# Kernel optimization log

Measured on AMD Instinct MI355X. Metric: run time of the kernel, lower is better.

The kernel has to match this reference:

```python
import jax, jax.numpy as jnp
import numpy as np
import math

B, S, E = 8, 128, 192
H = 6
HD = E // H  # 32
L = 64       # latent_dim (hardcoded default in MHLA)
N_EXP = 8
TOP_K = 2
ED = 768     # expert_dim
EPS = 1e-5


def setup_inputs() -> dict:
    key = jax.random.key(0)
    ks = jax.random.split(key, 24)
    sc = 0.02
    nrm = lambda k, shp: (jax.random.normal(k, shp, dtype=jnp.float32) * sc)
    inp = {
        "x": jax.random.normal(ks[0], (B, S, E), dtype=jnp.float32),
        "rms1_w": jnp.ones((E,), jnp.float32),
        "rms2_w": jnp.ones((E,), jnp.float32),
        # latent_tokens: Linear(S*E -> L*E); stored [in, out]
        "latW": nrm(ks[1], (S * E, L * E)),
        "latb": jnp.zeros((L * E,), jnp.float32),
        "qW": nrm(ks[2], (E, E)), "qb": jnp.zeros((E,), jnp.float32),
        "kW": nrm(ks[3], (E, E)), "kb": jnp.zeros((E,), jnp.float32),
        "vW": nrm(ks[4], (E, E)), "vb": jnp.zeros((E,), jnp.float32),
        "oW": nrm(ks[5], (E, E)), "ob": jnp.zeros((E,), jnp.float32),
        "rW": nrm(ks[6], (E, N_EXP)), "rb": jnp.zeros((N_EXP,), jnp.float32),
        # stacked expert params: layer1 (E->ED), swiglu-linear (ED->ED), layer2 (ED->E)
        "e1W": nrm(ks[7], (N_EXP, E, ED)), "e1b": jnp.zeros((N_EXP, ED), jnp.float32),
        "swW": nrm(ks[8], (N_EXP, ED, ED)), "swb": jnp.zeros((N_EXP, ED), jnp.float32),
        "e2W": nrm(ks[9], (N_EXP, ED, E)), "e2b": jnp.zeros((N_EXP, E), jnp.float32),
    }
    return inp


def _rmsnorm(x, w):
    ms = jnp.mean(x * x, axis=-1, keepdims=True)
    return x * jax.lax.rsqrt(ms + EPS) * w


def _rope_q(q):
    # q: [B,H,S,HD]; rotate interleaved pairs, torch-style view(..., HD//2, 2)
    t = jnp.arange(S, dtype=jnp.float32)
    inv_freq = 1.0 / (10000.0 ** (jnp.arange(0, HD, 2, dtype=jnp.float32) / HD))
    freqs = jnp.outer(t, inv_freq)            # [S, HD/2]
    cos, sin = jnp.cos(freqs), jnp.sin(freqs)
    qp = q.reshape(B, H, S, HD // 2, 2)
    x1, x2 = qp[..., 0], qp[..., 1]
    r1 = x1 * cos - x2 * sin
    r2 = x1 * sin + x2 * cos
    return jnp.stack([r1, r2], axis=-1).reshape(B, H, S, HD)


def _mhla(x, latW, latb, qW, qb, kW, kb, vW, vb, oW, ob):
    latent = (x.reshape(B, S * E) @ latW + latb).reshape(B, L, E)
    q = (x @ qW + qb).reshape(B, S, H, HD).transpose(0, 2, 1, 3)       # [B,H,S,HD]
    k = (latent @ kW + kb).reshape(B, L, H, HD).transpose(0, 2, 1, 3)  # [B,H,L,HD]
    v = (latent @ vW + vb).reshape(B, L, H, HD).transpose(0, 2, 1, 3)
    qr = _rope_q(q)  # RoPE applied to query only (key_r = key in source)
    scores = jnp.einsum("bhsd,bhld->bhsl", qr, k) / math.sqrt(HD)
    attn = jax.nn.softmax(scores, axis=-1)
    out = jnp.einsum("bhsl,bhld->bhsd", attn, v)
    out = out.transpose(0, 2, 1, 3).reshape(B, S, E)
    return out @ oW + ob


def _moe(h, rW, rb, e1W, e1b, swW, swb, e2W, e2b):
    probs = jax.nn.softmax(h @ rW + rb, axis=-1)          # [B,S,N]
    pk, idx = jax.lax.top_k(probs, TOP_K)                 # [B,S,K]
    # dense all-expert compute (8 small experts), then gather top-k
    t1 = jnp.einsum("bse,neh->bsnh", h, e1W) + e1b        # [B,S,N,ED]
    t2 = jax.nn.relu(jnp.einsum("bsnh,nhg->bsng", t1, swW) + swb)
    eo = jnp.einsum("bsng,nge->bsne", t2, e2W) + e2b      # [B,S,N,E]
    sel = jnp.take_along_axis(eo, idx[..., None], axis=2) # [B,S,K,E]
    return jnp.sum(pk[..., None] * sel, axis=2)


def reference(x, rms1_w, rms2_w, latW, latb, qW, qb, kW, kb, vW, vb, oW, ob,
              rW, rb, e1W, e1b, swW, swb, e2W, e2b):
    x = x + _mhla(_rmsnorm(x, rms1_w), latW, latb, qW, qb, kW, kb, vW, vb, oW, ob)
    x = x + _moe(_rmsnorm(x, rms2_w), rW, rb, e1W, e1b, swW, swb, e2W, e2b)
    return x
```

## Files before the change

### kernel.cpp

```cpp
#include <hip/hip_runtime.h>
#include <hip/hip_bf16.h>
#include <math.h>

#define B 8
#define S 128
#define E 192
#define H 6
#define HD 32
#define L 64
#define NEXP 8
#define ED 768
#define T (B*S)
#define SE (S*E)
#define LE (L*E)

#define SPLITS 64
#define ISPAN 384
#define CHUNK 128

using s8 = __attribute__((ext_vector_type(8))) short;
using f4 = __attribute__((ext_vector_type(4))) float;

__global__ __launch_bounds__(64) void rmsnorm_k(const float* __restrict__ x,
                                                const float* __restrict__ w,
                                                float* __restrict__ y) {
  int row = blockIdx.x;
  int lane = threadIdx.x;
  const float* xr = x + (size_t)row * E;
  float v0 = xr[lane], v1 = xr[lane + 64], v2 = xr[lane + 128];
  float s = v0 * v0 + v1 * v1 + v2 * v2;
#pragma unroll
  for (int off = 32; off > 0; off >>= 1) s += __shfl_xor(s, off);
  float inv = rsqrtf(s * (1.0f / E) + 1e-5f);
  float* yr = y + (size_t)row * E;
  yr[lane]       = v0 * inv * w[lane];
  yr[lane + 64]  = v1 * inv * w[lane + 64];
  yr[lane + 128] = v2 * inv * w[lane + 128];
}

__global__ __launch_bounds__(256) void lat_partial_k(const float* __restrict__ xn,
                                                     const float* __restrict__ latW,
                                                     float* __restrict__ part) {
  const int tid = threadIdx.x;
  const int j = blockIdx.x * 1024 + tid * 4;
  const int i0 = blockIdx.y * ISPAN;
  __shared__ float xs[CHUNK][8];
  f4 acc[8];
#pragma unroll
  for (int b = 0; b < 8; ++b) acc[b] = (f4){0.f, 0.f, 0.f, 0.f};
  for (int c = 0; c < ISPAN; c += CHUNK) {
    float* xsf = (float*)xs;
    __syncthreads();
    for (int l = tid; l < CHUNK * 8; l += 256) {
      int ii = l >> 3, b = l & 7;
      xsf[l] = xn[(size_t)b * SE + i0 + c + ii];
    }
    __syncthreads();
#pragma unroll 8
    for (int ii = 0; ii < CHUNK; ++ii) {
      const f4 w = __builtin_nontemporal_load(
          (const f4*)&latW[(size_t)(i0 + c + ii) * LE + j]);
#pragma unroll
      for (int b = 0; b < 8; ++b) {
        float xv = xs[ii][b];
        acc[b][0] += xv * w[0];
        acc[b][1] += xv * w[1];
        acc[b][2] += xv * w[2];
        acc[b][3] += xv * w[3];
      }
    }
  }
#pragma unroll
  for (int b = 0; b < 8; ++b)
    *(f4*)&part[((size_t)blockIdx.y * 8 + b) * LE + j] = acc[b];
}

__global__ __launch_bounds__(256) void lat_reduce_k(const float* __restrict__ part,
                                                    const float* __restrict__ latb,
                                                    float* __restrict__ lat) {
  int g = blockIdx.x * 256 + threadIdx.x;
  int b = g / LE, j = g - b * LE;
  float s = latb[j];
  for (int sp = 0; sp < SPLITS; ++sp) s += part[((size_t)sp * 8 + b) * LE + j];
  lat[g] = s;
}

__global__ __launch_bounds__(256) void qkv_k(const float* __restrict__ xn,
                                             const float* __restrict__ lat,
                                             const float* __restrict__ qW, const float* __restrict__ qb,
                                             const float* __restrict__ kW, const float* __restrict__ kb,
                                             const float* __restrict__ vW, const float* __restrict__ vb,
                                             float* __restrict__ qo,
                                             float* __restrict__ ko,
                                             float* __restrict__ vo) {
  const int z = blockIdx.z;
  const float* A = (z == 0) ? xn : lat;
  const float* W = (z == 0) ? qW : (z == 1) ? kW : vW;
  const float* bp = (z == 0) ? qb : (z == 1) ? kb : vb;
  float* C = (z == 0) ? qo : (z == 1) ? ko : vo;
  const int M = (z == 0) ? T : (B * L);
  const int m0 = blockIdx.y * 64;
  if (m0 >= M) return;
  const int n0 = blockIdx.x * 64;
  __shared__ float As[16][64];
  __shared__ float Ws[16][64];
  const int tid = threadIdx.x;
  const int tx = tid & 15, ty = tid >> 4;
  const int arow = tid >> 2, acol = (tid & 3) << 2;
  const int wrow = tid >> 4, wcol = (tid & 15) << 2;
  float acc[4][4] = {{0.f}};
  for (int kb2 = 0; kb2 < E; kb2 += 16) {
    float4 a = *(const float4*)&A[(size_t)(m0 + arow) * E + kb2 + acol];
    As[acol][arow] = a.x;
    As[acol + 1][arow] = a.y;
    As[acol + 2][arow] = a.z;
    As[acol + 3][arow] = a.w;
    *(float4*)&Ws[wrow][wcol] = *(const float4*)&W[(size_t)(kb2 + wrow) * E + n0 + wcol];
    __syncthreads();
#pragma unroll
    for (int k = 0; k < 16; ++k) {
      float4 a4 = *(const float4*)&As[k][ty << 2];
      float4 w4 = *(const float4*)&Ws[k][tx << 2];
      acc[0][0] += a4.x * w4.x; acc[0][1] += a4.x * w4.y; acc[0][2] += a4.x * w4.z; acc[0][3] += a4.x * w4.w;
      acc[1][0] += a4.y * w4.x; acc[1][1] += a4.y * w4.y; acc[1][2] += a4.y * w4.z; acc[1][3] += a4.y * w4.w;
      acc[2][0] += a4.z * w4.x; acc[2][1] += a4.z * w4.y; acc[2][2] += a4.z * w4.z; acc[2][3] += a4.z * w4.w;
      acc[3][0] += a4.w * w4.x; acc[3][1] += a4.w * w4.y; acc[3][2] += a4.w * w4.z; acc[3][3] += a4.w * w4.w;
    }
    __syncthreads();
  }
#pragma unroll
  for (int i = 0; i < 4; ++i) {
    int m = m0 + (ty << 2) + i;
#pragma unroll
    for (int jj = 0; jj < 4; ++jj) {
      int n = n0 + (tx << 2) + jj;
      C[(size_t)m * E + n] = acc[i][jj] + bp[n];
    }
  }
}

__global__ __launch_bounds__(256) void gemm_k(const float* __restrict__ A,
                                              const float* __restrict__ W,
                                              const float* __restrict__ bias,
                                              const float* __restrict__ resid,
                                              float* __restrict__ C,
                                              int M, int N, int K,
                                              int flags) {
  const int n0 = blockIdx.x * 64;
  const int m0 = blockIdx.y * 64;
  __shared__ float As[16][64];
  __shared__ float Ws[16][64];
  const int tid = threadIdx.x;
  const int tx = tid & 15, ty = tid >> 4;
  const int arow = tid >> 2, acol = (tid & 3) << 2;
  const int wrow = tid >> 4, wcol = (tid & 15) << 2;
  float acc[4][4] = {{0.f}};
  for (int kb = 0; kb < K; kb += 16) {
    float4 a = *(const float4*)&A[(size_t)(m0 + arow) * K + kb + acol];
    As[acol][arow] = a.x;
    As[acol + 1][arow] = a.y;
    As[acol + 2][arow] = a.z;
    As[acol + 3][arow] = a.w;
    *(float4*)&Ws[wrow][wcol] = *(const float4*)&W[(size_t)(kb + wrow) * N + n0 + wcol];
    __syncthreads();
#pragma unroll
    for (int k = 0; k < 16; ++k) {
      float4 a4 = *(const float4*)&As[k][ty << 2];
      float4 w4 = *(const float4*)&Ws[k][tx << 2];
      acc[0][0] += a4.x * w4.x; acc[0][1] += a4.x * w4.y; acc[0][2] += a4.x * w4.z; acc[0][3] += a4.x * w4.w;
      acc[1][0] += a4.y * w4.x; acc[1][1] += a4.y * w4.y; acc[1][2] += a4.y * w4.z; acc[1][3] += a4.y * w4.w;
      acc[2][0] += a4.z * w4.x; acc[2][1] += a4.z * w4.y; acc[2][2] += a4.z * w4.z; acc[2][3] += a4.z * w4.w;
      acc[3][0] += a4.w * w4.x; acc[3][1] += a4.w * w4.y; acc[3][2] += a4.w * w4.z; acc[3][3] += a4.w * w4.w;
    }
    __syncthreads();
  }
#pragma unroll
  for (int i = 0; i < 4; ++i) {
    int m = m0 + (ty << 2) + i;
#pragma unroll
    for (int j = 0; j < 4; ++j) {
      int n = n0 + (tx << 2) + j;
      float v = acc[i][j];
      if (bias) v += bias[n];
      if (flags & 1) v = fmaxf(v, 0.f);
      if (flags & 2) v += resid[(size_t)m * N + n];
      C[(size_t)m * N + n] = v;
    }
  }
}

__global__ __launch_bounds__(256) void tconv_k(const float* __restrict__ in,
                                               __hip_bfloat16* __restrict__ out,
                                               int K, int N) {
  const int e = blockIdx.z;
  in += (size_t)e * K * N;
  out += (size_t)e * N * K;
  __shared__ float tile[32][33];
  int tx = threadIdx.x & 31, r8 = threadIdx.x >> 5;
  int k0 = blockIdx.x * 32, n0 = blockIdx.y * 32;
#pragma unroll
  for (int i = 0; i < 4; ++i)
    tile[r8 + 8 * i][tx] = in[(size_t)(k0 + r8 + 8 * i) * N + n0 + tx];
  __syncthreads();
#pragma unroll
  for (int i = 0; i < 4; ++i) {
    int nr = r8 + 8 * i;
    out[(size_t)(n0 + nr) * K + k0 + tx] = __float2bfloat16(tile[tx][nr]);
  }
}

__global__ __launch_bounds__(64) void router_rms_k(const float* __restrict__ x1,
                                                   const float* __restrict__ w,
                                                   const float* __restrict__ rW,
                                                   const float* __restrict__ rb,
                                                   __hip_bfloat16* __restrict__ hb,
                                                   float* __restrict__ pk,
                                                   int* __restrict__ idx) {
  int t = blockIdx.x;
  int lane = threadIdx.x;
  const float* xr = x1 + (size_t)t * E;
  float v0 = xr[lane], v1 = xr[lane + 64], v2 = xr[lane + 128];
  float s = v0 * v0 + v1 * v1 + v2 * v2;
#pragma unroll
  for (int off = 32; off > 0; off >>= 1) s += __shfl_xor(s, off);
  float inv = rsqrtf(s * (1.0f / E) + 1e-5f);
  float r0 = v0 * inv * w[lane];
  float r1 = v1 * inv * w[lane + 64];
  float r2 = v2 * inv * w[lane + 128];
  __hip_bfloat16* yrb = hb + (size_t)t * E;
  yrb[lane] = __float2bfloat16(r0);
  yrb[lane + 64] = __float2bfloat16(r1);
  yrb[lane + 128] = __float2bfloat16(r2);
  float lg[8];
#pragma unroll
  for (int n = 0; n < 8; ++n)
    lg[n] = r0 * rW[lane * 8 + n] + r1 * rW[(lane + 64) * 8 + n] + r2 * rW[(lane + 128) * 8 + n];
#pragma unroll
  for (int n = 0; n < 8; ++n)
#pragma unroll
    for (int off = 32; off > 0; off >>= 1) lg[n] += __shfl_xor(lg[n], off);
  if (lane == 0) {
#pragma unroll
    for (int n = 0; n < 8; ++n) lg[n] += rb[n];
    float mx = lg[0];
#pragma unroll
    for (int n = 1; n < 8; ++n) mx = fmaxf(mx, lg[n]);
    float p[8], sum = 0.f;
#pragma unroll
    for (int n = 0; n < 8; ++n) { p[n] = __expf(lg[n] - mx); sum += p[n]; }
    float isum = 1.f / sum;
#pragma unroll
    for (int n = 0; n < 8; ++n) p[n] *= isum;
    int i0 = 0;
#pragma unroll
    for (int n = 1; n < 8; ++n) if (p[n] > p[i0]) i0 = n;
    int i1 = (i0 == 0) ? 1 : 0;
#pragma unroll
    for (int n = 0; n < 8; ++n) if (n != i0 && p[n] > p[i1]) i1 = n;
    pk[t * 2] = p[i0];
    pk[t * 2 + 1] = p[i1];
    idx[t * 2] = i0;
    idx[t * 2 + 1] = i1;
  }
}

__global__ __launch_bounds__(512) void compact_k(const int* __restrict__ idx,
                                                 int* __restrict__ toklist,
                                                 int* __restrict__ ppos,
                                                 int* __restrict__ cnt) {
  int e = threadIdx.x >> 6;
  int lane = threadIdx.x & 63;
  int pos = 0;
  for (int base = 0; base < T; base += 64) {
    int t = base + lane;
    int i0 = idx[t * 2], i1 = idx[t * 2 + 1];
    bool sel = (i0 == e) || (i1 == e);
    unsigned long long m = __ballot(sel);
    int myoff = __popcll(m & ((1ull << lane) - 1ull));
    if (sel) {
      int p = pos + myoff;
      toklist[e * T + p] = t;
      ppos[t * 2 + ((i0 == e) ? 0 : 1)] = p;
    }
    pos += __popcll(m);
  }
  if (lane == 0) cnt[e] = pos;
}

__global__ __launch_bounds__(256) void moe_gemm_g(const __hip_bfloat16* __restrict__ A_,
                                                  const __hip_bfloat16* __restrict__ Wt_,
                                                  const float* __restrict__ bias_,
                                                  void* __restrict__ C_,
                                                  const int* __restrict__ toklist,
                                                  const int* __restrict__ cntp,
                                                  int N, int K,
                                                  long aB, long wB, long bB, long cB,
                                                  int flags) {
  const int e = blockIdx.z;
  const int cnt = cntp[e];
  const int m0 = blockIdx.y * 128;
  if (m0 >= cnt) return;
  const short* A = (const short*)A_ + ((flags & 4) ? 0 : (size_t)e * aB);
  const short* Wt = (const short*)Wt_ + (size_t)e * wB;
  const float* bias = bias_ + (size_t)e * bB;
  const int n0 = blockIdx.x * 64;
  __shared__ short As[128 * 64];
  __shared__ short Bs[64 * 64];
  const int tid = threadIdx.x;
  const int lane = tid & 63, wid = tid >> 6;
  const int wr = wid >> 1, wc = wid & 1;
  const int lr = lane & 15, lg = lane >> 4;
  long arow_off[4];
#pragma unroll
  for (int p = 0; p < 4; ++p) {
    int row = p * 32 + (tid >> 3);
    int gr = m0 + row;
    int src;
    if (flags & 4) src = (gr < cnt) ? toklist[e * T + gr] : toklist[e * T];
    else src = gr;
    arow_off[p] = (size_t)src * K;
  }
  f4 acc[4][2];
#pragma unroll
  for (int fm = 0; fm < 4; ++fm)
#pragma unroll
    for (int fn = 0; fn < 2; ++fn) acc[fm][fn] = (f4){0.f, 0.f, 0.f, 0.f};

  const int slot = tid & 7;
  for (int kb = 0; kb < K; kb += 64) {
    __syncthreads();
#pragma unroll
    for (int p = 0; p < 4; ++p) {
      int row = p * 32 + (tid >> 3);
      s8 v = *(const s8*)(A + arow_off[p] + kb + slot * 8);
      *(s8*)&As[row * 64 + ((slot ^ (row & 7)) << 3)] = v;
    }
#pragma unroll
    for (int p = 0; p < 2; ++p) {
      int row = p * 32 + (tid >> 3);
      s8 v = *(const s8*)(Wt + (size_t)(n0 + row) * K + kb + slot * 8);
      *(s8*)&Bs[row * 64 + ((slot ^ (row & 7)) << 3)] = v;
    }
    __syncthreads();
#pragma unroll
    for (int kk = 0; kk < 64; kk += 32) {
      const int sb = (kk >> 3) + lg;
      s8 af[4], bf[2];
#pragma unroll
      for (int fm = 0; fm < 4; ++fm) {
        int row = wr * 64 + fm * 16 + lr;
        af[fm] = *(const s8*)&As[row * 64 + ((sb ^ (row & 7)) << 3)];
      }
#pragma unroll
      for (int fn = 0; fn < 2; ++fn) {
        int row = wc * 32 + fn * 16 + lr;
        bf[fn] = *(const s8*)&Bs[row * 64 + ((sb ^ (row & 7)) << 3)];
      }
#pragma unroll
      for (int fm = 0; fm < 4; ++fm)
#pragma unroll
        for (int fn = 0; fn < 2; ++fn)
          acc[fm][fn] = __builtin_amdgcn_mfma_f32_16x16x32_bf16(af[fm], bf[fn], acc[fm][fn], 0, 0, 0);
    }
  }
#pragma unroll
  for (int fm = 0; fm < 4; ++fm) {
#pragma unroll
    for (int fn = 0; fn < 2; ++fn) {
      int col = n0 + wc * 32 + fn * 16 + lr;
      int rowb = m0 + wr * 64 + fm * 16 + lg * 4;
      float bv = bias[col];
#pragma unroll
      for (int j = 0; j < 4; ++j) {
        if (rowb + j >= cnt) continue;
        float v = acc[fm][fn][j] + bv;
        if (flags & 1) v = fmaxf(v, 0.f);
        if (flags & 2)
          ((float*)C_)[(size_t)e * cB + (size_t)(rowb + j) * N + col] = v;
        else
          ((__hip_bfloat16*)C_)[(size_t)e * cB + (size_t)(rowb + j) * N + col] = __float2bfloat16(v);
      }
    }
  }
}

__global__ __launch_bounds__(128) void attn_k(const float* __restrict__ q,
                                              const float* __restrict__ kk,
                                              const float* __restrict__ vv,
                                              float* __restrict__ ao) {
  int b = blockIdx.x / H, h = blockIdx.x % H;
  __shared__ float ks[64][32], vs[64][32];
  int tid = threadIdx.x;
  {
    int l = tid >> 1, hf = (tid & 1) * 16;
    const float4* ksrc = (const float4*)&kk[(size_t)(b * L + l) * E + h * HD + hf];
    const float4* vsrc = (const float4*)&vv[(size_t)(b * L + l) * E + h * HD + hf];
    float4* kdst = (float4*)&ks[l][hf];
    float4* vdst = (float4*)&vs[l][hf];
#pragma unroll
    for (int u = 0; u < 4; ++u) { kdst[u] = ksrc[u]; vdst[u] = vsrc[u]; }
  }
  __syncthreads();
  int s = tid;
  const float* qp = &q[(size_t)(b * S + s) * E + h * HD];
  float qv[32];
#pragma unroll
  for (int d = 0; d < 32; ++d) qv[d] = qp[d];
#pragma unroll
  for (int d = 0; d < 16; ++d) {
    float invf = exp2f(-(float)d * (13.287712379549449f / 16.0f));
    float ang = (float)s * invf;
    float sn, cs;
    __sincosf(ang, &sn, &cs);
    float x1 = qv[2 * d], x2 = qv[2 * d + 1];
    qv[2 * d] = x1 * cs - x2 * sn;
    qv[2 * d + 1] = x1 * sn + x2 * cs;
  }
  const float scale = 0.17677669529663687f;
  float mx = -1e30f;
  for (int l = 0; l < 64; ++l) {
    float dot = 0.f;
#pragma unroll
    for (int d = 0; d < 32; ++d) dot += qv[d] * ks[l][d];
    mx = fmaxf(mx, dot * scale);
  }
  float o[32];
#pragma unroll
  for (int d = 0; d < 32; ++d) o[d] = 0.f;
  float sum = 0.f;
  for (int l = 0; l < 64; ++l) {
    float dot = 0.f;
#pragma unroll
    for (int d = 0; d < 32; ++d) dot += qv[d] * ks[l][d];
    float wgt = __expf(dot * scale - mx);
    sum += wgt;
#pragma unroll
    for (int d = 0; d < 32; ++d) o[d] += wgt * vs[l][d];
  }
  float inv = 1.0f / sum;
  float* op = &ao[(size_t)(b * S + s) * E + h * HD];
#pragma unroll
  for (int d = 0; d < 32; ++d) op[d] = o[d] * inv;
}

__global__ __launch_bounds__(256) void combine_k(const float* __restrict__ x1,
                                                 const float* __restrict__ eoc,
                                                 const float* __restrict__ pk,
                                                 const int* __restrict__ idx,
                                                 const int* __restrict__ ppos,
                                                 float* __restrict__ out) {
  int g = blockIdx.x * 256 + threadIdx.x;
  int t = g / E;
  int e = g - t * E;
  int i0 = idx[t * 2], i1 = idx[t * 2 + 1];
  int p0 = ppos[t * 2], p1 = ppos[t * 2 + 1];
  out[g] = x1[g] + pk[t * 2] * eoc[((size_t)i0 * T + p0) * E + e]
                 + pk[t * 2 + 1] * eoc[((size_t)i1 * T + p1) * E + e];
}

extern "C" void kernel_launch(void* const* d_in, const int* in_sizes, int n_in,
                              void* d_out, int out_size, void* d_ws, size_t ws_size,
                              hipStream_t stream) {
  const float* x    = (const float*)d_in[0];
  const float* r1w  = (const float*)d_in[1];
  const float* r2w  = (const float*)d_in[2];
  const float* latW = (const float*)d_in[3];
  const float* latb = (const float*)d_in[4];
  const float* qW   = (const float*)d_in[5];
  const float* qb   = (const float*)d_in[6];
  const float* kW   = (const float*)d_in[7];
  const float* kb   = (const float*)d_in[8];
  const float* vW   = (const float*)d_in[9];
  const float* vb   = (const float*)d_in[10];
  const float* oW   = (const float*)d_in[11];
  const float* ob   = (const float*)d_in[12];
  const float* rW   = (const float*)d_in[13];
  const float* rb   = (const float*)d_in[14];
  const float* e1W  = (const float*)d_in[15];
  const float* e1b  = (const float*)d_in[16];
  const float* swW  = (const float*)d_in[17];
  const float* swb  = (const float*)d_in[18];
  const float* e2W  = (const float*)d_in[19];
  const float* e2b  = (const float*)d_in[20];
  float* out = (float*)d_out;

  float* ws = (float*)d_ws;
  float* xn1  = ws;
  float* lat  = ws + 196608;
  float* qbuf = ws + 294912;
  float* kbuf = ws + 491520;
  float* vbuf = ws + 589824;
  float* ao   = ws + 688128;
  float* x1   = ws + 884736;
  float* pk   = ws + 1277952;
  int*   idx  = (int*)(ws + 1280000);
  int*   toklist = (int*)(ws + 1282048);
  int*   ppos    = (int*)(ws + 1290240);
  int*   cnt     = (int*)(ws + 1292288);
  __hip_bfloat16* hb    = (__hip_bfloat16*)(ws + 1294336);
  __hip_bfloat16* e1Wt  = (__hip_bfloat16*)(ws + 1392640);
  __hip_bfloat16* swWt  = (__hip_bfloat16*)(ws + 1982464);
  __hip_bfloat16* e2Wt  = (__hip_bfloat16*)(ws + 4341760);
  __hip_bfloat16* t1    = (__hip_bfloat16*)(ws + 4931584);
  __hip_bfloat16* t2    = (__hip_bfloat16*)(ws + 8077312);
  float* eoc  = ws + 11223040;
  float* part = ws + 12795904;

  tconv_k<<<dim3(E / 32, ED / 32, NEXP), 256, 0, stream>>>(e1W, e1Wt, E, ED);
  tconv_k<<<dim3(ED / 32, ED / 32, NEXP), 256, 0, stream>>>(swW, swWt, ED, ED);
  tconv_k<<<dim3(ED / 32, E / 32, NEXP), 256, 0, stream>>>(e2W, e2Wt, ED, E);

  rmsnorm_k<<<T, 64, 0, stream>>>(x, r1w, xn1);
  lat_partial_k<<<dim3(12, SPLITS), 256, 0, stream>>>(xn1, latW, part);
  lat_reduce_k<<<(8 * LE) / 256, 256, 0, stream>>>(part, latb, lat);
  qkv_k<<<dim3(3, 16, 3), 256, 0, stream>>>(xn1, lat, qW, qb, kW, kb, vW, vb,
                                            qbuf, kbuf, vbuf);
  attn_k<<<B * H, 128, 0, stream>>>(qbuf, kbuf, vbuf, ao);
  gemm_k<<<dim3(3, 16), 256, 0, stream>>>(ao, oW, ob, x, x1, T, E, E, 2);
  router_rms_k<<<T, 64, 0, stream>>>(x1, r2w, rW, rb, hb, pk, idx);
  compact_k<<<1, 512, 0, stream>>>(idx, toklist, ppos, cnt);
  moe_gemm_g<<<dim3(ED / 64, 8, NEXP), 256, 0, stream>>>(
      hb, e1Wt, e1b, t1, toklist, cnt, ED, E, 0, (long)ED * E, ED, (long)T * ED, 4);
  moe_gemm_g<<<dim3(ED / 64, 8, NEXP), 256, 0, stream>>>(
      t1, swWt, swb, t2, toklist, cnt, ED, ED, (long)T * ED, (long)ED * ED, ED, (long)T * ED, 1);
  moe_gemm_g<<<dim3(E / 64, 8, NEXP), 256, 0, stream>>>(
      t2, e2Wt, e2b, eoc, toklist, cnt, E, ED, (long)T * ED, (long)E * ED, E, (long)T * E, 2);
  combine_k<<<(T * E) / 256, 256, 0, stream>>>(x1, eoc, pk, idx, ppos, out);
}
```

Before: 340.4 us.

## Move QKV and output projections to bf16 MFMA kernels

Replaces the fp32 scalar-FMA QKV and output-projection GEMMs with bf16 MFMA kernels that use swizzled LDS tiles. The producing kernels now also emit bf16 copies: the rmsnorm output, the latent and the attention output. A new kernel transposes and converts the four projection weights to bf16 on every call. This targets the compute cost of the small attention GEMMs, but these are a small share of the total (the latent GEMM and the MoE dominate), and it adds bf16 rounding error plus an extra conversion launch.

Measured after the change: 322.3 us. -5.3%, faster.

```diff
diff --git a/kernel.cpp b/kernel.cpp
--- a/kernel.cpp
+++ b/kernel.cpp
@@ -21,9 +21,10 @@
 using s8 = __attribute__((ext_vector_type(8))) short;
 using f4 = __attribute__((ext_vector_type(4))) float;
 
-__global__ __launch_bounds__(64) void rmsnorm_k(const float* __restrict__ x,
-                                                const float* __restrict__ w,
-                                                float* __restrict__ y) {
+__global__ __launch_bounds__(64) void rmsnorm_bf_k(const float* __restrict__ x,
+                                                   const float* __restrict__ w,
+                                                   float* __restrict__ y,
+                                                   __hip_bfloat16* __restrict__ yb) {
   int row = blockIdx.x;
   int lane = threadIdx.x;
   const float* xr = x + (size_t)row * E;
@@ -32,10 +33,15 @@
 #pragma unroll
   for (int off = 32; off > 0; off >>= 1) s += __shfl_xor(s, off);
   float inv = rsqrtf(s * (1.0f / E) + 1e-5f);
+  float r0 = v0 * inv * w[lane];
+  float r1 = v1 * inv * w[lane + 64];
+  float r2 = v2 * inv * w[lane + 128];
   float* yr = y + (size_t)row * E;
-  yr[lane]       = v0 * inv * w[lane];
-  yr[lane + 64]  = v1 * inv * w[lane + 64];
-  yr[lane + 128] = v2 * inv * w[lane + 128];
+  __hip_bfloat16* yrb = yb + (size_t)row * E;
+  yr[lane] = r0; yr[lane + 64] = r1; yr[lane + 128] = r2;
+  yrb[lane] = __float2bfloat16(r0);
+  yrb[lane + 64] = __float2bfloat16(r1);
+  yrb[lane + 128] = __float2bfloat16(r2);
 }
 
 __global__ __launch_bounds__(256) void lat_partial_k(const float* __restrict__ xn,
@@ -77,115 +83,36 @@
 
 __global__ __launch_bounds__(256) void lat_reduce_k(const float* __restrict__ part,
                                                     const float* __restrict__ latb,
-                                                    float* __restrict__ lat) {
+                                                    __hip_bfloat16* __restrict__ lat16) {
   int g = blockIdx.x * 256 + threadIdx.x;
   int b = g / LE, j = g - b * LE;
   float s = latb[j];
   for (int sp = 0; sp < SPLITS; ++sp) s += part[((size_t)sp * 8 + b) * LE + j];
-  lat[g] = s;
-}
-
-__global__ __launch_bounds__(256) void qkv_k(const float* __restrict__ xn,
-                                             const float* __restrict__ lat,
-                                             const float* __restrict__ qW, const float* __restrict__ qb,
-                                             const float* __restrict__ kW, const float* __restrict__ kb,
-                                             const float* __restrict__ vW, const float* __restrict__ vb,
-                                             float* __restrict__ qo,
-                                             float* __restrict__ ko,
-                                             float* __restrict__ vo) {
+  lat16[g] = __float2bfloat16(s);
+}
+
+__global__ __launch_bounds__(256) void tconv4_k(const float* __restrict__ qW,
+                                                const float* __restrict__ kW,
+                                                const float* __restrict__ vW,
+                                                const float* __restrict__ oW,
+                                                __hip_bfloat16* __restrict__ qWt,
+                                                __hip_bfloat16* __restrict__ kWt,
+                                                __hip_bfloat16* __restrict__ vWt,
+                                                __hip_bfloat16* __restrict__ oWt) {
   const int z = blockIdx.z;
-  const float* A = (z == 0) ? xn : lat;
-  const float* W = (z == 0) ? qW : (z == 1) ? kW : vW;
-  const float* bp = (z == 0) ? qb : (z == 1) ? kb : vb;
-  float* C = (z == 0) ? qo : (z == 1) ? ko : vo;
-  const int M = (z == 0) ? T : (B * L);
-  const int m0 = blockIdx.y * 64;
-  if (m0 >= M) return;
-  const int n0 = blockIdx.x * 64;
-  __shared__ float As[16][64];
-  __shared__ float Ws[16][64];
-  const int tid = threadIdx.x;
-  const int tx = tid & 15, ty = tid >> 4;
-  const int arow = tid >> 2, acol = (tid & 3) << 2;
-  const int wrow = tid >> 4, wcol = (tid & 15) << 2;
-  float acc[4][4] = {{0.f}};
-  for (int kb2 = 0; kb2 < E; kb2 += 16) {
-    float4 a = *(const float4*)&A[(size_t)(m0 + arow) * E + kb2 + acol];
-    As[acol][arow] = a.x;
-    As[acol + 1][arow] = a.y;
-    As[acol + 2][arow] = a.z;
-    As[acol + 3][arow] = a.w;
-    *(float4*)&Ws[wrow][wcol] = *(const float4*)&W[(size_t)(kb2 + wrow) * E + n0 + wcol];
-    __syncthreads();
-#pragma unroll
-    for (int k = 0; k < 16; ++k) {
-      float4 a4 = *(const float4*)&As[k][ty << 2];
-      float4 w4 = *(const float4*)&Ws[k][tx << 2];
-      acc[0][0] += a4.x * w4.x; acc[0][1] += a4.x * w4.y; acc[0][2] += a4.x * w4.z; acc[0][3] += a4.x * w4.w;
-      acc[1][0] += a4.y * w4.x; acc[1][1] += a4.y * w4.y; acc[1][2] += a4.y * w4.z; acc[1][3] += a4.y * w4.w;
-      acc[2][0] += a4.z * w4.x; acc[2][1] += a4.z * w4.y; acc[2][2] += a4.z * w4.z; acc[2][3] += a4.z * w4.w;
-      acc[3][0] += a4.w * w4.x; acc[3][1] += a4.w * w4.y; acc[3][2] += a4.w * w4.z; acc[3][3] += a4.w * w4.w;
-    }
-    __syncthreads();
-  }
+  const float* in = (z == 0) ? qW : (z == 1) ? kW : (z == 2) ? vW : oW;
+  __hip_bfloat16* out = (z == 0) ? qWt : (z == 1) ? kWt : (z == 2) ? vWt : oWt;
+  __shared__ float tile[32][33];
+  int tx = threadIdx.x & 31, r8 = threadIdx.x >> 5;
+  int k0 = blockIdx.x * 32, n0 = blockIdx.y * 32;
+#pragma unroll
+  for (int i = 0; i < 4; ++i)
+    tile[r8 + 8 * i][tx] = in[(size_t)(k0 + r8 + 8 * i) * E + n0 + tx];
+  __syncthreads();
 #pragma unroll
   for (int i = 0; i < 4; ++i) {
-    int m = m0 + (ty << 2) + i;
-#pragma unroll
-    for (int jj = 0; jj < 4; ++jj) {
-      int n = n0 + (tx << 2) + jj;
-      C[(size_t)m * E + n] = acc[i][jj] + bp[n];
-    }
-  }
-}
-
-__global__ __launch_bounds__(256) void gemm_k(const float* __restrict__ A,
-                                              const float* __restrict__ W,
-                                              const float* __restrict__ bias,
-                                              const float* __restrict__ resid,
-                                              float* __restrict__ C,
-                                              int M, int N, int K,
-                                              int flags) {
-  const int n0 = blockIdx.x * 64;
-  const int m0 = blockIdx.y * 64;
-  __shared__ float As[16][64];
-  __shared__ float Ws[16][64];
-  const int tid = threadIdx.x;
-  const int tx = tid & 15, ty = tid >> 4;
-  const int arow = tid >> 2, acol = (tid & 3) << 2;
-  const int wrow = tid >> 4, wcol = (tid & 15) << 2;
-  float acc[4][4] = {{0.f}};
-  for (int kb = 0; kb < K; kb += 16) {
-    float4 a = *(const float4*)&A[(size_t)(m0 + arow) * K + kb + acol];
-    As[acol][arow] = a.x;
-    As[acol + 1][arow] = a.y;
-    As[acol + 2][arow] = a.z;
-    As[acol + 3][arow] = a.w;
-    *(float4*)&Ws[wrow][wcol] = *(const float4*)&W[(size_t)(kb + wrow) * N + n0 + wcol];
-    __syncthreads();
-#pragma unroll
-    for (int k = 0; k < 16; ++k) {
-      float4 a4 = *(const float4*)&As[k][ty << 2];
-      float4 w4 = *(const float4*)&Ws[k][tx << 2];
-      acc[0][0] += a4.x * w4.x; acc[0][1] += a4.x * w4.y; acc[0][2] += a4.x * w4.z; acc[0][3] += a4.x * w4.w;
-      acc[1][0] += a4.y * w4.x; acc[1][1] += a4.y * w4.y; acc[1][2] += a4.y * w4.z; acc[1][3] += a4.y * w4.w;
-      acc[2][0] += a4.z * w4.x; acc[2][1] += a4.z * w4.y; acc[2][2] += a4.z * w4.z; acc[2][3] += a4.z * w4.w;
-      acc[3][0] += a4.w * w4.x; acc[3][1] += a4.w * w4.y; acc[3][2] += a4.w * w4.z; acc[3][3] += a4.w * w4.w;
-    }
-    __syncthreads();
-  }
-#pragma unroll
-  for (int i = 0; i < 4; ++i) {
-    int m = m0 + (ty << 2) + i;
-#pragma unroll
-    for (int j = 0; j < 4; ++j) {
-      int n = n0 + (tx << 2) + j;
-      float v = acc[i][j];
-      if (bias) v += bias[n];
-      if (flags & 1) v = fmaxf(v, 0.f);
-      if (flags & 2) v += resid[(size_t)m * N + n];
-      C[(size_t)m * N + n] = v;
-    }
+    int nr = r8 + 8 * i;
+    out[(size_t)(n0 + nr) * E + k0 + tx] = __float2bfloat16(tile[tx][nr]);
   }
 }
 
@@ -207,6 +134,159 @@
     int nr = r8 + 8 * i;
     out[(size_t)(n0 + nr) * K + k0 + tx] = __float2bfloat16(tile[tx][nr]);
   }
+}
+
+__global__ __launch_bounds__(256) void qkv_mm_k(const __hip_bfloat16* __restrict__ xnb,
+                                                const __hip_bfloat16* __restrict__ lat16,
+                                                const __hip_bfloat16* __restrict__ qWt,
+                                                const __hip_bfloat16* __restrict__ kWt,
+                                                const __hip_bfloat16* __restrict__ vWt,
+                                                const float* __restrict__ qb,
+                                                const float* __restrict__ kb,
+                                                const float* __restrict__ vb,
+                                                float* __restrict__ qo,
+                                                float* __restrict__ ko,
+                                                float* __restrict__ vo) {
+  const int z = blockIdx.z;
+  const int M = (z == 0) ? T : (B * L);
+  const int m0 = blockIdx.y * 128;
+  if (m0 >= M) return;
+  const short* A = (const short*)((z == 0) ? xnb : lat16);
+  const short* Wt = (const short*)((z == 0) ? qWt : (z == 1) ? kWt : vWt);
+  const float* bias = (z == 0) ? qb : (z == 1) ? kb : vb;
+  float* C = (z == 0) ? qo : (z == 1) ? ko : vo;
+  const int n0 = blockIdx.x * 64;
+  __shared__ short As[128 * 64];
+  __shared__ short Bs[64 * 64];
+  const int tid = threadIdx.x;
+  const int lane = tid & 63, wid = tid >> 6;
+  const int wr = wid >> 1, wc = wid & 1;
+  const int lr = lane & 15, lg = lane >> 4;
+  const int slot = tid & 7;
+  f4 acc[4][2];
+#pragma unroll
+  for (int fm = 0; fm < 4; ++fm)
+#pragma unroll
+    for (int fn = 0; fn < 2; ++fn) acc[fm][fn] = (f4){0.f, 0.f, 0.f, 0.f};
+  for (int kb2 = 0; kb2 < E; kb2 += 64) {
+    __syncthreads();
+#pragma unroll
+    for (int p = 0; p < 4; ++p) {
+      int row = p * 32 + (tid >> 3);
+      s8 v = *(const s8*)(A + (size_t)(m0 + row) * E + kb2 + slot * 8);
+      *(s8*)&As[row * 64 + ((slot ^ (row & 7)) << 3)] = v;
+    }
+#pragma unroll
+    for (int p = 0; p < 2; ++p) {
+      int row = p * 32 + (tid >> 3);
+      s8 v = *(const s8*)(Wt + (size_t)(n0 + row) * E + kb2 + slot * 8);
+      *(s8*)&Bs[row * 64 + ((slot ^ (row & 7)) << 3)] = v;
+    }
+    __syncthreads();
+#pragma unroll
+    for (int kk = 0; kk < 64; kk += 32) {
+      const int sb = (kk >> 3) + lg;
+      s8 af[4], bf[2];
+#pragma unroll
+      for (int fm = 0; fm < 4; ++fm) {
+        int row = wr * 64 + fm * 16 + lr;
+        af[fm] = *(const s8*)&As[row * 64 + ((sb ^ (row & 7)) << 3)];
+      }
+#pragma unroll
+      for (int fn = 0; fn < 2; ++fn) {
+        int row = wc * 32 + fn * 16 + lr;
+        bf[fn] = *(const s8*)&Bs[row * 64 + ((sb ^ (row & 7)) << 3)];
+      }
+#pragma unroll
+      for (int fm = 0; fm < 4; ++fm)
+#pragma unroll
+        for (int fn = 0; fn < 2; ++fn)
+          acc[fm][fn] = __builtin_amdgcn_mfma_f32_16x16x32_bf16(af[fm], bf[fn], acc[fm][fn], 0, 0, 0);
+    }
+  }
+#pragma unroll
+  for (int fm = 0; fm < 4; ++fm)
+#pragma unroll
+    for (int fn = 0; fn < 2; ++fn) {
+      int col = n0 + wc * 32 + fn * 16 + lr;
+      int rowb = m0 + wr * 64 + fm * 16 + lg * 4;
+      float bv = bias[col];
+#pragma unroll
+      for (int j = 0; j < 4; ++j)
+        C[(size_t)(rowb + j) * E + col] = acc[fm][fn][j] + bv;
+    }
+}
+
+__global__ __launch_bounds__(256) void oproj_mm_k(const __hip_bfloat16* __restrict__ aob,
+                                                  const __hip_bfloat16* __restrict__ oWt,
+                                                  const float* __restrict__ ob,
+                                                  const float* __restrict__ x,
+                                                  float* __restrict__ x1) {
+  const int m0 = blockIdx.y * 128;
+  const int n0 = blockIdx.x * 64;
+  const short* A = (const short*)aob;
+  const short* Wt = (const short*)oWt;
+  __shared__ short As[128 * 64];
+  __shared__ short Bs[64 * 64];
+  const int tid = threadIdx.x;
+  const int lane = tid & 63, wid = tid >> 6;
+  const int wr = wid >> 1, wc = wid & 1;
+  const int lr = lane & 15, lg = lane >> 4;
+  const int slot = tid & 7;
+  f4 acc[4][2];
+#pragma unroll
+  for (int fm = 0; fm < 4; ++fm)
+#pragma unroll
+    for (int fn = 0; fn < 2; ++fn) acc[fm][fn] = (f4){0.f, 0.f, 0.f, 0.f};
+  for (int kb2 = 0; kb2 < E; kb2 += 64) {
+    __syncthreads();
+#pragma unroll
+    for (int p = 0; p < 4; ++p) {
+      int row = p * 32 + (tid >> 3);
+      s8 v = *(const s8*)(A + (size_t)(m0 + row) * E + kb2 + slot * 8);
+      *(s8*)&As[row * 64 + ((slot ^ (row & 7)) << 3)] = v;
+    }
+#pragma unroll
+    for (int p = 0; p < 2; ++p) {
+      int row = p * 32 + (tid >> 3);
+      s8 v = *(const s8*)(Wt + (size_t)(n0 + row) * E + kb2 + slot * 8);
+      *(s8*)&Bs[row * 64 + ((slot ^ (row & 7)) << 3)] = v;
+    }
+    __syncthreads();
+#pragma unroll
+    for (int kk = 0; kk < 64; kk += 32) {
+      const int sb = (kk >> 3) + lg;
+      s8 af[4], bf[2];
+#pragma unroll
+      for (int fm = 0; fm < 4; ++fm) {
+        int row = wr * 64 + fm * 16 + lr;
+        af[fm] = *(const s8*)&As[row * 64 + ((sb ^ (row & 7)) << 3)];
+      }
+#pragma unroll
+      for (int fn = 0; fn < 2; ++fn) {
+        int row = wc * 32 + fn * 16 + lr;
+        bf[fn] = *(const s8*)&Bs[row * 64 + ((sb ^ (row & 7)) << 3)];
+      }
+#pragma unroll
+      for (int fm = 0; fm < 4; ++fm)
+#pragma unroll
+        for (int fn = 0; fn < 2; ++fn)
+          acc[fm][fn] = __builtin_amdgcn_mfma_f32_16x16x32_bf16(af[fm], bf[fn], acc[fm][fn], 0, 0, 0);
+    }
+  }
+#pragma unroll
+  for (int fm = 0; fm < 4; ++fm)
+#pragma unroll
+    for (int fn = 0; fn < 2; ++fn) {
+      int col = n0 + wc * 32 + fn * 16 + lr;
+      int rowb = m0 + wr * 64 + fm * 16 + lg * 4;
+      float bv = ob[col];
+#pragma unroll
+      for (int j = 0; j < 4; ++j) {
+        size_t off = (size_t)(rowb + j) * E + col;
+        x1[off] = acc[fm][fn][j] + bv + x[off];
+      }
+    }
 }
 
 __global__ __launch_bounds__(64) void router_rms_k(const float* __restrict__ x1,
@@ -325,7 +405,6 @@
   for (int fm = 0; fm < 4; ++fm)
 #pragma unroll
     for (int fn = 0; fn < 2; ++fn) acc[fm][fn] = (f4){0.f, 0.f, 0.f, 0.f};
-
   const int slot = tid & 7;
   for (int kb = 0; kb < K; kb += 64) {
     __syncthreads();
@@ -387,7 +466,7 @@
 __global__ __launch_bounds__(128) void attn_k(const float* __restrict__ q,
                                               const float* __restrict__ kk,
                                               const float* __restrict__ vv,
-                                              float* __restrict__ ao) {
+                                              __hip_bfloat16* __restrict__ aob) {
   int b = blockIdx.x / H, h = blockIdx.x % H;
   __shared__ float ks[64][32], vs[64][32];
   int tid = threadIdx.x;
@@ -438,9 +517,9 @@
     for (int d = 0; d < 32; ++d) o[d] += wgt * vs[l][d];
   }
   float inv = 1.0f / sum;
-  float* op = &ao[(size_t)(b * S + s) * E + h * HD];
-#pragma unroll
-  for (int d = 0; d < 32; ++d) op[d] = o[d] * inv;
+  __hip_bfloat16* op = &aob[(size_t)(b * S + s) * E + h * HD];
+#pragma unroll
+  for (int d = 0; d < 32; ++d) op[d] = __float2bfloat16(o[d] * inv);
 }
 
 __global__ __launch_bounds__(256) void combine_k(const float* __restrict__ x1,
@@ -486,37 +565,43 @@
 
   float* ws = (float*)d_ws;
   float* xn1  = ws;
-  float* lat  = ws + 196608;
-  float* qbuf = ws + 294912;
-  float* kbuf = ws + 491520;
-  float* vbuf = ws + 589824;
-  float* ao   = ws + 688128;
-  float* x1   = ws + 884736;
-  float* pk   = ws + 1277952;
-  int*   idx  = (int*)(ws + 1280000);
-  int*   toklist = (int*)(ws + 1282048);
-  int*   ppos    = (int*)(ws + 1290240);
-  int*   cnt     = (int*)(ws + 1292288);
-  __hip_bfloat16* hb    = (__hip_bfloat16*)(ws + 1294336);
-  __hip_bfloat16* e1Wt  = (__hip_bfloat16*)(ws + 1392640);
-  __hip_bfloat16* swWt  = (__hip_bfloat16*)(ws + 1982464);
-  __hip_bfloat16* e2Wt  = (__hip_bfloat16*)(ws + 4341760);
-  __hip_bfloat16* t1    = (__hip_bfloat16*)(ws + 4931584);
-  __hip_bfloat16* t2    = (__hip_bfloat16*)(ws + 8077312);
-  float* eoc  = ws + 11223040;
-  float* part = ws + 12795904;
+  __hip_bfloat16* xnb   = (__hip_bfloat16*)(ws + 196608);
+  __hip_bfloat16* lat16 = (__hip_bfloat16*)(ws + 294912);
+  float* qbuf = ws + 344064;
+  float* kbuf = ws + 540672;
+  float* vbuf = ws + 638976;
+  __hip_bfloat16* aob   = (__hip_bfloat16*)(ws + 737280);
+  float* x1   = ws + 835584;
+  float* pk   = ws + 1032192;
+  int*   idx  = (int*)(ws + 1034240);
+  int*   toklist = (int*)(ws + 1036288);
+  int*   ppos    = (int*)(ws + 1044480);
+  int*   cnt     = (int*)(ws + 1046528);
+  __hip_bfloat16* qWt = (__hip_bfloat16*)(ws + 1046784);
+  __hip_bfloat16* kWt = (__hip_bfloat16*)(ws + 1065216);
+  __hip_bfloat16* vWt = (__hip_bfloat16*)(ws + 1083648);
+  __hip_bfloat16* oWt = (__hip_bfloat16*)(ws + 1102080);
+  __hip_bfloat16* hb    = (__hip_bfloat16*)(ws + 1120512);
+  __hip_bfloat16* e1Wt  = (__hip_bfloat16*)(ws + 1218816);
+  __hip_bfloat16* swWt  = (__hip_bfloat16*)(ws + 1808640);
+  __hip_bfloat16* e2Wt  = (__hip_bfloat16*)(ws + 4167936);
+  __hip_bfloat16* t1    = (__hip_bfloat16*)(ws + 4757760);
+  __hip_bfloat16* t2    = (__hip_bfloat16*)(ws + 7903488);
+  float* eoc  = ws + 11049216;
+  float* part = ws + 12622080;
 
   tconv_k<<<dim3(E / 32, ED / 32, NEXP), 256, 0, stream>>>(e1W, e1Wt, E, ED);
   tconv_k<<<dim3(ED / 32, ED / 32, NEXP), 256, 0, stream>>>(swW, swWt, ED, ED);
   tconv_k<<<dim3(ED / 32, E / 32, NEXP), 256, 0, stream>>>(e2W, e2Wt, ED, E);
-
-  rmsnorm_k<<<T, 64, 0, stream>>>(x, r1w, xn1);
+  tconv4_k<<<dim3(6, 6, 4), 256, 0, stream>>>(qW, kW, vW, oW, qWt, kWt, vWt, oWt);
+
+  rmsnorm_bf_k<<<T, 64, 0, stream>>>(x, r1w, xn1, xnb);
   lat_partial_k<<<dim3(12, SPLITS), 256, 0, stream>>>(xn1, latW, part);
-  lat_reduce_k<<<(8 * LE) / 256, 256, 0, stream>>>(part, latb, lat);
-  qkv_k<<<dim3(3, 16, 3), 256, 0, stream>>>(xn1, lat, qW, qb, kW, kb, vW, vb,
-                                            qbuf, kbuf, vbuf);
-  attn_k<<<B * H, 128, 0, stream>>>(qbuf, kbuf, vbuf, ao);
-  gemm_k<<<dim3(3, 16), 256, 0, stream>>>(ao, oW, ob, x, x1, T, E, E, 2);
+  lat_reduce_k<<<(8 * LE) / 256, 256, 0, stream>>>(part, latb, lat16);
+  qkv_mm_k<<<dim3(3, 8, 3), 256, 0, stream>>>(xnb, lat16, qWt, kWt, vWt,
+                                              qb, kb, vb, qbuf, kbuf, vbuf);
+  attn_k<<<B * H, 128, 0, stream>>>(qbuf, kbuf, vbuf, aob);
+  oproj_mm_k<<<dim3(3, 8), 256, 0, stream>>>(aob, oWt, ob, x, x1);
   router_rms_k<<<T, 64, 0, stream>>>(x1, r2w, rW, rb, hb, pk, idx);
   compact_k<<<1, 512, 0, stream>>>(idx, toklist, ppos, cnt);
   moe_gemm_g<<<dim3(ED / 64, 8, NEXP), 256, 0, stream>>>(
```
